# Performance work log

Measured on AMD Instinct MI355X. Metric: run time of the kernel, lower is better.

The kernel has to match this reference:

```python
import jax, jax.numpy as jnp
import numpy as np

# RasterConfig constants
H, W = 192, 192
FRONT_K = 8
ALPHA_THRESH = 1.0 / 255.0
ALPHA_CLAMP = 0.999  # standard gsplat clamp to keep transmittance > 0
BG = jnp.array([0.0, 0.0, 0.0], dtype=jnp.float32)
B, G = 1, 1024


def setup_inputs() -> dict:
    key = jax.random.key(0)
    k0, k1, k2, k3, k4, k5, k6 = jax.random.split(key, 7)
    # pixel-space means covering the image
    means2d = jax.random.uniform(k0, (B, G, 2), dtype=jnp.float32) * jnp.array([W, H], dtype=jnp.float32)
    # positive-definite inverse covariance (a, b, c): b^2 < a*c
    a = jax.random.uniform(k1, (B, G), dtype=jnp.float32, minval=0.02, maxval=0.25)
    c = jax.random.uniform(k2, (B, G), dtype=jnp.float32, minval=0.02, maxval=0.25)
    b = (jax.random.uniform(k3, (B, G), dtype=jnp.float32, minval=-1.0, maxval=1.0) * 0.5) * jnp.sqrt(a * c)
    conics = jnp.stack([a, b, c], axis=-1)
    colors = jax.random.uniform(k4, (B, G, 3), dtype=jnp.float32)
    opacities = jax.random.uniform(k5, (B, G), dtype=jnp.float32, minval=0.2, maxval=1.0)
    depths = jax.random.uniform(k6, (B, G), dtype=jnp.float32, minval=0.1, maxval=10.0)
    return {"means2d": means2d, "conics": conics, "colors": colors,
            "opacities": opacities, "depths": depths}


def _rasterize(means2d, conics, colors, opacities, depths):
    b, g, _ = means2d.shape
    # depth sort: front (smallest depth) to back
    order = jnp.argsort(depths, axis=1)                       # [B,G] int
    m = jnp.take_along_axis(means2d, order[..., None], axis=1)    # [B,G,2]
    con = jnp.take_along_axis(conics, order[..., None], axis=1)   # [B,G,3]
    col = jnp.take_along_axis(colors, order[..., None], axis=1)   # [B,G,3]
    op = jnp.take_along_axis(opacities, order, axis=1)            # [B,G]

    # pixel centers, flattened [HW]
    xs = jnp.arange(W, dtype=jnp.float32) + 0.5
    ys = jnp.arange(H, dtype=jnp.float32) + 0.5
    pgx, pgy = jnp.meshgrid(xs, ys)                           # [H,W]
    px = pgx.reshape(-1)
    py = pgy.reshape(-1)

    dx = px[None, None, :] - m[..., 0][..., None]             # [B,G,HW]
    dy = py[None, None, :] - m[..., 1][..., None]             # [B,G,HW]
    A = con[..., 0][..., None]
    Bc = con[..., 1][..., None]
    Cc = con[..., 2][..., None]
    sigma = 0.5 * (A * dx * dx + Cc * dy * dy) + Bc * dx * dy  # [B,G,HW]
    alpha = jnp.minimum(op[..., None] * jnp.exp(-sigma), ALPHA_CLAMP)

    # skip invalid (sigma<0) or sub-threshold gaussians
    valid = (sigma >= 0.0) & (alpha >= ALPHA_THRESH)
    # front-k truncation: only first K contributing gaussians per pixel
    rank = jnp.cumsum(valid.astype(jnp.int32), axis=1)
    contrib = valid & (rank <= FRONT_K)
    a_eff = jnp.where(contrib, alpha, 0.0)                    # [B,G,HW]

    # front-to-back alpha compositing
    T = jnp.cumprod(1.0 - a_eff, axis=1)                      # inclusive transmittance
    T_excl = jnp.concatenate([jnp.ones_like(T[:, :1]), T[:, :-1]], axis=1)
    w = T_excl * a_eff                                        # per-gaussian weight [B,G,HW]
    img = jnp.einsum('bgp,bgc->bpc', w, col)                  # [B,HW,3]
    img = img + T[:, -1, :][..., None] * BG                   # composite background
    return img.reshape(b, H, W, 3)


def reference(means2d, conics, colors, opacities, depths):
    return _rasterize(means2d, conics, colors, opacities, depths)
```

## Files before the change

kernel.cpp:

```cpp
#include <hip/hip_runtime.h>

#define IMG_H 192
#define IMG_W 192
#define NG    1024
#define TILE  8
#define TX    24
#define TY    24
#define FRONT_K 8
#define ALPHA_THRESH (1.0f / 255.0f)
#define ALPHA_CLAMP  0.999f
#define CAP   64

__global__ __launch_bounds__(64) void raster_fused(
    const float* __restrict__ means2d, const float* __restrict__ conics,
    const float* __restrict__ colors,  const float* __restrict__ opac,
    const float* __restrict__ depths,  float* __restrict__ out)
{
    __shared__ unsigned short cg[NG];
    __shared__ float          cd[NG];
    __shared__ unsigned short sg[NG];
    __shared__ float4 gA[CAP];
    __shared__ float4 gB[CAP];
    __shared__ float2 gC[CAP];

    const int lane = threadIdx.x;
    const int tx = blockIdx.x % TX;
    const int ty = blockIdx.x / TX;

    const float px0 = (float)(tx * TILE) + 0.5f;
    const float px1 = px0 + (float)(TILE - 1);
    const float py0 = (float)(ty * TILE) + 0.5f;
    const float py1 = py0 + (float)(TILE - 1);

    int n = 0;
    for (int c = 0; c < NG / 64; ++c) {
        const int g = c * 64 + lane;
        const float mx = means2d[2 * g + 0];
        const float my = means2d[2 * g + 1];
        const float ca = conics[3 * g + 0];
        const float cb = conics[3 * g + 1];
        const float cc = conics[3 * g + 2];
        const float op = opac[g];
        const float thr = __logf(255.0f * op) + 1e-3f;
        const float det = ca * cc - cb * cb;
        bool hit = false;
        if (thr > 0.0f && det > 0.0f) {
            const float hx = sqrtf(2.0f * thr * cc / det) + 0.01f;
            const float hy = sqrtf(2.0f * thr * ca / det) + 0.01f;
            hit = (mx - hx <= px1) && (mx + hx >= px0) &&
                  (my - hy <= py1) && (my + hy >= py0);
        }
        const unsigned long long m = __ballot(hit);
        if (hit) {
            const int pos = n + __popcll(m & ((1ull << lane) - 1ull));
            cg[pos] = (unsigned short)g;
            cd[pos] = depths[g];
        }
        n += __popcll(m);
    }
    __syncthreads();

    for (int r = lane; r < n; r += 64) {
        const float dr = cd[r];
        const int   gr = cg[r];
        int rank = 0;
        for (int j = 0; j < n; ++j) {
            const float dj = cd[j];
            rank += (dj < dr) || (dj == dr && cg[j] < gr);
        }
        sg[rank] = (unsigned short)gr;
    }
    __syncthreads();

    const int col = lane & 7, row = lane >> 3;
    const float px = px0 + (float)col;
    const float py = py0 + (float)row;

    float T = 1.0f, accr = 0.0f, accg = 0.0f, accb = 0.0f;
    int cnt = 0;

    for (int start = 0; start < n; start += CAP) {
        const int m2 = min(CAP, n - start);
        if (lane < m2) {
            const int g = sg[start + lane];
            const float mx = means2d[2 * g + 0];
            const float my = means2d[2 * g + 1];
            const float ca = conics[3 * g + 0];
            const float cb = conics[3 * g + 1];
            const float cc = conics[3 * g + 2];
            const float op = opac[g];
            const float thr = __logf(255.0f * op) + 1e-3f;
            gA[lane] = make_float4(mx, my, ca, cb);
            gB[lane] = make_float4(cc, thr, op, colors[3 * g + 0]);
            gC[lane] = make_float2(colors[3 * g + 1], colors[3 * g + 2]);
        }
        __syncthreads();

        for (int i = 0; i < m2; ++i) {
            const float4 A  = gA[i];
            const float4 Bv = gB[i];
            const float dx = px - A.x;
            const float dy = py - A.y;
            const float sigma = 0.5f * (A.z * dx * dx + Bv.x * dy * dy)
                              + A.w * dx * dy;
            if (sigma >= 0.0f && sigma <= Bv.y && cnt < FRONT_K) {
                float alpha = Bv.z * __expf(-sigma);
                if (alpha >= ALPHA_THRESH) {
                    alpha = fminf(alpha, ALPHA_CLAMP);
                    const float w = T * alpha;
                    const float2 C = gC[i];
                    accr += w * Bv.w;
                    accg += w * C.x;
                    accb += w * C.y;
                    T *= (1.0f - alpha);
                    ++cnt;
                }
            }
            if ((i & 7) == 7 && __all(cnt >= FRONT_K)) { start = NG; break; }
        }
        __syncthreads();
        if (__all(cnt >= FRONT_K)) break;
    }

    const int pix = (ty * TILE + row) * IMG_W + (tx * TILE + col);
    out[pix * 3 + 0] = accr;
    out[pix * 3 + 1] = accg;
    out[pix * 3 + 2] = accb;
}

extern "C" void kernel_launch(void* const* d_in, const int* in_sizes, int n_in,
                              void* d_out, int out_size, void* d_ws, size_t ws_size,
                              hipStream_t stream)
{
    const float* means2d = (const float*)d_in[0];
    const float* conics  = (const float*)d_in[1];
    const float* colors  = (const float*)d_in[2];
    const float* opac    = (const float*)d_in[3];
    const float* depths  = (const float*)d_in[4];

    (void)d_ws; (void)ws_size;

    raster_fused<<<TX * TY, 64, 0, stream>>>(
        means2d, conics, colors, opac, depths, (float*)d_out);
}
```

Measured before the change: 83.60 us.

## Share culling and depth sort across four 8x8 tiles per 256-thread block

```diff
diff --git a/kernel.cpp b/kernel.cpp
--- a/kernel.cpp
+++ b/kernel.cpp
@@ -4,14 +4,14 @@
 #define IMG_W 192
 #define NG    1024
 #define TILE  8
-#define TX    24
-#define TY    24
+#define QTX   12
+#define QTY   12
 #define FRONT_K 8
 #define ALPHA_THRESH (1.0f / 255.0f)
 #define ALPHA_CLAMP  0.999f
 #define CAP   64
 
-__global__ __launch_bounds__(64) void raster_fused(
+__global__ __launch_bounds__(256) void raster_fused(
     const float* __restrict__ means2d, const float* __restrict__ conics,
     const float* __restrict__ colors,  const float* __restrict__ opac,
     const float* __restrict__ depths,  float* __restrict__ out)
@@ -19,48 +19,61 @@
     __shared__ unsigned short cg[NG];
     __shared__ float          cd[NG];
     __shared__ unsigned short sg[NG];
+    __shared__ int            wcnt[4];
     __shared__ float4 gA[CAP];
     __shared__ float4 gB[CAP];
     __shared__ float2 gC[CAP];
 
-    const int lane = threadIdx.x;
-    const int tx = blockIdx.x % TX;
-    const int ty = blockIdx.x / TX;
+    const int tid  = threadIdx.x;
+    const int lane = tid & 63;
+    const int wid  = tid >> 6;
+    const int qx = blockIdx.x % QTX;
+    const int qy = blockIdx.x / QTX;
 
-    const float px0 = (float)(tx * TILE) + 0.5f;
-    const float px1 = px0 + (float)(TILE - 1);
-    const float py0 = (float)(ty * TILE) + 0.5f;
-    const float py1 = py0 + (float)(TILE - 1);
+    const float rx0 = (float)(qx * 16) + 0.5f;
+    const float rx1 = rx0 + 15.0f;
+    const float ry0 = (float)(qy * 16) + 0.5f;
+    const float ry1 = ry0 + 15.0f;
 
     int n = 0;
-    for (int c = 0; c < NG / 64; ++c) {
-        const int g = c * 64 + lane;
+    #pragma unroll
+    for (int c = 0; c < NG / 256; ++c) {
+        const int g = c * 256 + tid;
         const float mx = means2d[2 * g + 0];
         const float my = means2d[2 * g + 1];
         const float ca = conics[3 * g + 0];
         const float cb = conics[3 * g + 1];
         const float cc = conics[3 * g + 2];
         const float op = opac[g];
+        const float dp = depths[g];
         const float thr = __logf(255.0f * op) + 1e-3f;
         const float det = ca * cc - cb * cb;
         bool hit = false;
         if (thr > 0.0f && det > 0.0f) {
             const float hx = sqrtf(2.0f * thr * cc / det) + 0.01f;
             const float hy = sqrtf(2.0f * thr * ca / det) + 0.01f;
-            hit = (mx - hx <= px1) && (mx + hx >= px0) &&
-                  (my - hy <= py1) && (my + hy >= py0);
+            hit = (mx - hx <= rx1) && (mx + hx >= rx0) &&
+                  (my - hy <= ry1) && (my + hy >= ry0);
         }
         const unsigned long long m = __ballot(hit);
+        if (lane == 0) wcnt[wid] = __popcll(m);
+        __syncthreads();
+        int ofs = n;
+        #pragma unroll
+        for (int w = 0; w < 4; ++w) {
+            if (w < wid) ofs += wcnt[w];
+        }
+        const int tot = wcnt[0] + wcnt[1] + wcnt[2] + wcnt[3];
         if (hit) {
-            const int pos = n + __popcll(m & ((1ull << lane) - 1ull));
+            const int pos = ofs + __popcll(m & ((1ull << lane) - 1ull));
             cg[pos] = (unsigned short)g;
-            cd[pos] = depths[g];
+            cd[pos] = dp;
         }
-        n += __popcll(m);
+        n += tot;
+        __syncthreads();
     }
-    __syncthreads();
 
-    for (int r = lane; r < n; r += 64) {
+    for (int r = tid; r < n; r += 256) {
         const float dr = cd[r];
         const int   gr = cg[r];
         int rank = 0;
@@ -72,17 +85,19 @@
     }
     __syncthreads();
 
+    const int tx = qx * 2 + (wid & 1);
+    const int ty = qy * 2 + (wid >> 1);
     const int col = lane & 7, row = lane >> 3;
-    const float px = px0 + (float)col;
-    const float py = py0 + (float)row;
+    const float px = (float)(tx * TILE + col) + 0.5f;
+    const float py = (float)(ty * TILE + row) + 0.5f;
 
     float T = 1.0f, accr = 0.0f, accg = 0.0f, accb = 0.0f;
     int cnt = 0;
 
     for (int start = 0; start < n; start += CAP) {
         const int m2 = min(CAP, n - start);
-        if (lane < m2) {
-            const int g = sg[start + lane];
+        if (tid < m2) {
+            const int g = sg[start + tid];
             const float mx = means2d[2 * g + 0];
             const float my = means2d[2 * g + 1];
             const float ca = conics[3 * g + 0];
@@ -90,36 +105,36 @@
             const float cc = conics[3 * g + 2];
             const float op = opac[g];
             const float thr = __logf(255.0f * op) + 1e-3f;
-            gA[lane] = make_float4(mx, my, ca, cb);
-            gB[lane] = make_float4(cc, thr, op, colors[3 * g + 0]);
-            gC[lane] = make_float2(colors[3 * g + 1], colors[3 * g + 2]);
+            gA[tid] = make_float4(mx, my, ca, cb);
+            gB[tid] = make_float4(cc, thr, op, colors[3 * g + 0]);
+            gC[tid] = make_float2(colors[3 * g + 1], colors[3 * g + 2]);
         }
         __syncthreads();
 
-        for (int i = 0; i < m2; ++i) {
-            const float4 A  = gA[i];
-            const float4 Bv = gB[i];
-            const float dx = px - A.x;
-            const float dy = py - A.y;
-            const float sigma = 0.5f * (A.z * dx * dx + Bv.x * dy * dy)
-                              + A.w * dx * dy;
-            if (sigma >= 0.0f && sigma <= Bv.y && cnt < FRONT_K) {
-                float alpha = Bv.z * __expf(-sigma);
-                if (alpha >= ALPHA_THRESH) {
-                    alpha = fminf(alpha, ALPHA_CLAMP);
-                    const float w = T * alpha;
-                    const float2 C = gC[i];
-                    accr += w * Bv.w;
-                    accg += w * C.x;
-                    accb += w * C.y;
-                    T *= (1.0f - alpha);
-                    ++cnt;
+        if (!__all(cnt >= FRONT_K)) {
+            for (int i = 0; i < m2; ++i) {
+                const float4 A  = gA[i];
+                const float4 Bv = gB[i];
+                const float dx = px - A.x;
+                const float dy = py - A.y;
+                const float sigma = 0.5f * (A.z * dx * dx + Bv.x * dy * dy)
+                                  + A.w * dx * dy;
+                if (sigma >= 0.0f && sigma <= Bv.y && cnt < FRONT_K) {
+                    float alpha = Bv.z * __expf(-sigma);
+                    if (alpha >= ALPHA_THRESH) {
+                        alpha = fminf(alpha, ALPHA_CLAMP);
+                        const float w = T * alpha;
+                        const float2 C = gC[i];
+                        accr += w * Bv.w;
+                        accg += w * C.x;
+                        accb += w * C.y;
+                        T *= (1.0f - alpha);
+                        ++cnt;
+                    }
                 }
             }
-            if ((i & 7) == 7 && __all(cnt >= FRONT_K)) { start = NG; break; }
         }
-        __syncthreads();
-        if (__all(cnt >= FRONT_K)) break;
+        if (__syncthreads_and(cnt >= FRONT_K)) break;
     }
 
     const int pix = (ty * TILE + row) * IMG_W + (tx * TILE + col);
@@ -140,6 +155,6 @@
 
     (void)d_ws; (void)ws_size;
 
-    raster_fused<<<TX * TY, 64, 0, stream>>>(
+    raster_fused<<<QTX * QTY, 256, 0, stream>>>(
         means2d, conics, colors, opac, depths, (float*)d_out);
 }
```

Measured after the change: 77.12 us. -7.7%, faster.
